# Performance work log

Measured on AMD Instinct MI355X. Metric: run time of the kernel, lower is better.

Reference implementation:

```python
import jax, jax.numpy as jnp
import numpy as np


def _lstm_step(h, c, x, W_ih, W_hh, b_ih, b_hh):
    # PyTorch gate order: i, f, g, o
    gates = x @ W_ih.T + b_ih + h @ W_hh.T + b_hh
    i, f, g, o = jnp.split(gates, 4, axis=-1)
    c = jax.nn.sigmoid(f) * c + jax.nn.sigmoid(i) * jnp.tanh(g)
    h = jax.nn.sigmoid(o) * jnp.tanh(c)
    return h, c


def setup_inputs() -> dict:
    key = jax.random.key(0)
    ks = jax.random.split(key, 12)
    B, T = 256, 256
    S, A, H, K = 64, 16, 512, 512
    D = S + A  # 80
    s = 1.0 / np.sqrt(H)
    u = lambda k, shape, sc: jax.random.uniform(k, shape, jnp.float32, -sc, sc)
    return {
        "traj": jax.random.normal(ks[0], (B, T, D), jnp.float32),
        "seq_len": T,
        "enc_W_ih": u(ks[1], (4 * H, D), s),
        "enc_W_hh": u(ks[2], (4 * H, H), s),
        "enc_b_ih": u(ks[3], (4 * H,), s),
        "enc_b_hh": u(ks[4], (4 * H,), s),
        "embeddings": jax.random.uniform(ks[5], (K, H), jnp.float32, -1.0 / K, 1.0 / K),
        "dec_W_ih": u(ks[6], (4 * H, D), s),
        "dec_W_hh": u(ks[7], (4 * H, H), s),
        "dec_b_ih": u(ks[8], (4 * H,), s),
        "dec_b_hh": u(ks[9], (4 * H,), s),
        "fc_W": u(ks[10], (D, H), s),
        "fc_b": u(ks[11], (D,), s),
    }


def reference(traj, seq_len, enc_W_ih, enc_W_hh, enc_b_ih, enc_b_hh,
              embeddings, dec_W_ih, dec_W_hh, dec_b_ih, dec_b_hh, fc_W, fc_b):
    B = traj.shape[0]
    H = enc_W_hh.shape[1]
    D = traj.shape[-1]

    # ---- Encoder: many-to-one LSTM, keep final hidden state ----
    def enc_step(carry, x_t):
        h, c = carry
        h, c = _lstm_step(h, c, x_t, enc_W_ih, enc_W_hh, enc_b_ih, enc_b_hh)
        return (h, c), None
    h0 = jnp.zeros((B, H), traj.dtype)
    (z, _), _ = jax.lax.scan(enc_step, (h0, h0), jnp.swapaxes(traj, 0, 1))

    # ---- Vector quantizer ----
    d = (jnp.sum(z * z, axis=1, keepdims=True)
         + jnp.sum(embeddings * embeddings, axis=1)
         - 2.0 * z @ embeddings.T)  # [B, K]
    idx = jnp.argmin(d, axis=1)
    quantized = embeddings[idx]  # [B, H]
    e_latent = jnp.mean((jax.lax.stop_gradient(quantized) - z) ** 2)
    q_latent = jnp.mean((quantized - jax.lax.stop_gradient(z)) ** 2)
    vq_loss = q_latent + 0.25 * e_latent

    def dec_step(carry, _):
        h, c, x = carry
        h, c = _lstm_step(h, c, x, dec_W_ih, dec_W_hh, dec_b_ih, dec_b_hh)
        y = h @ fc_W.T + fc_b
        return (h, c, y), y
    x0 = jnp.zeros((B, D), traj.dtype)
    c0 = jnp.zeros((B, H), traj.dtype)
    _, ys = jax.lax.scan(dec_step, (quantized, c0, x0), None, length=seq_len)
    recon = jnp.swapaxes(ys, 0, 1)  # [B, seq_len, D]
    return recon, vq_loss, idx[:, None]
```

## Files before the change

kernel.cpp:

```cpp
#include <hip/hip_runtime.h>
#include <math.h>

#define BB 256
#define TT 256
#define DDIM 80
#define HDIM 512
#define ROWSTRIDE 20480

#define WS_HA    0
#define WS_CD    131072
#define WS_BAR   262144
#define WS_HB    263168
#define WS_QUANT 394240
#define WS_VQP   525312
#define WS_BENC  525568
#define WS_BDEC0 527616
#define WS_BEFF  529664
#define WS_WEFF  531712

typedef _Float16 f16;
typedef f16 half4_t __attribute__((ext_vector_type(4)));
typedef f16 half8_t __attribute__((ext_vector_type(8)));
typedef float float4_t __attribute__((ext_vector_type(4)));

__device__ __forceinline__ float sigmoidf_(float v) { return 1.0f / (1.0f + expf(-v)); }

__device__ __forceinline__ void llc_store_f32(float* p, float v) {
  asm volatile("global_store_dword %0, %1, off sc0 sc1" :: "v"(p), "v"(v) : "memory");
}
__device__ __forceinline__ void llc_store_i32(int* p, int v) {
  asm volatile("global_store_dword %0, %1, off sc0 sc1" :: "v"(p), "v"(v) : "memory");
}
__device__ __forceinline__ int llc_load_i32(const int* p) {
  int v;
  asm volatile("global_load_dword %0, %1, off sc0 sc1\n\ts_waitcnt vmcnt(0)"
               : "=v"(v) : "v"(p) : "memory");
  return v;
}
__device__ __forceinline__ void wait_vm0() {
  asm volatile("s_waitcnt vmcnt(0)" ::: "memory");
}
__device__ __forceinline__ void llc_load_4xf4_cols(
    const float4* base,
    float4& a0, float4& a1, float4& a2, float4& a3) {
  asm volatile(
      "global_load_dwordx4 %0, %4, off sc0 sc1\n\t"
      "global_load_dwordx4 %1, %5, off sc0 sc1\n\t"
      "global_load_dwordx4 %2, %6, off sc0 sc1\n\t"
      "global_load_dwordx4 %3, %7, off sc0 sc1\n\t"
      "s_waitcnt vmcnt(0)"
      : "=&v"(a0), "=&v"(a1), "=&v"(a2), "=&v"(a3)
      : "v"(base), "v"(base + 32), "v"(base + 64), "v"(base + 96)
      : "memory");
}

__global__ __launch_bounds__(256) void zero_kernel(float4* __restrict__ p, int n4) {
  int i = blockIdx.x * 256 + threadIdx.x;
  if (i < n4) p[i] = make_float4(0.f, 0.f, 0.f, 0.f);
}

__global__ __launch_bounds__(256) void bias_init_kernel(
    const float* __restrict__ eb1, const float* __restrict__ eb2,
    const float* __restrict__ db1, const float* __restrict__ db2,
    const float* __restrict__ dWih, const float* __restrict__ fcb,
    float* __restrict__ b_enc, float* __restrict__ b_dec0,
    float* __restrict__ b_eff) {
  int n = blockIdx.x * 256 + threadIdx.x;
  b_enc[n] = eb1[n] + eb2[n];
  float bd = db1[n] + db2[n];
  b_dec0[n] = bd;
  float acc = bd;
  #pragma unroll 16
  for (int d = 0; d < DDIM; d++) acc += dWih[n * DDIM + d] * fcb[d];
  b_eff[n] = acc;
}

__global__ __launch_bounds__(256) void fold_kernel(
    const float* __restrict__ dWih, const float* __restrict__ dWhh,
    const float* __restrict__ fcW, float* __restrict__ W_eff) {
  int n = blockIdx.x;
  int tid = threadIdx.x;
  __shared__ float sw[DDIM];
  if (tid < DDIM) sw[tid] = dWih[n * DDIM + tid];
  __syncthreads();
  for (int k = tid; k < HDIM; k += 256) {
    float acc = dWhh[n * HDIM + k];
    #pragma unroll 16
    for (int d = 0; d < DDIM; d++) acc += sw[d] * fcW[d * HDIM + k];
    W_eff[n * HDIM + k] = acc;
  }
}

__global__ __launch_bounds__(256) void lstm_step_kernel(
    const float* __restrict__ Whh, const float* __restrict__ bias,
    const float* __restrict__ h_in, float* __restrict__ c,
    float* __restrict__ h_out) {
  __shared__ float sh[16][516];
  int tid = threadIdx.x;
  int rt = blockIdx.x & 15, jt = blockIdx.x >> 4;
  int row0 = rt << 4;
  for (int i = tid; i < 2048; i += 256) {
    int r = i >> 7, kq = i & 127;
    float4 v = *(const float4*)(h_in + (size_t)(row0 + r) * HDIM + (kq << 2));
    *(float4*)&sh[r][kq << 2] = v;
  }
  __syncthreads();
  int r = tid & 15, j0 = tid >> 4;
  int j = (jt << 4) + j0;
  float a0 = bias[j], a1 = bias[512 + j], a2 = bias[1024 + j], a3 = bias[1536 + j];
  const float4* w0 = (const float4*)(Whh + (size_t)j * HDIM);
  const float4* w1 = (const float4*)(Whh + (size_t)(512 + j) * HDIM);
  const float4* w2 = (const float4*)(Whh + (size_t)(1024 + j) * HDIM);
  const float4* w3 = (const float4*)(Whh + (size_t)(1536 + j) * HDIM);
  const float4* hv = (const float4*)&sh[r][0];
  #pragma unroll 4
  for (int kq = 0; kq < 128; kq++) {
    float4 h4 = hv[kq];
    float4 q0 = w0[kq], q1 = w1[kq], q2 = w2[kq], q3 = w3[kq];
    a0 += h4.x * q0.x + h4.y * q0.y + h4.z * q0.z + h4.w * q0.w;
    a1 += h4.x * q1.x + h4.y * q1.y + h4.z * q1.z + h4.w * q1.w;
    a2 += h4.x * q2.x + h4.y * q2.y + h4.z * q2.z + h4.w * q2.w;
    a3 += h4.x * q3.x + h4.y * q3.y + h4.z * q3.z + h4.w * q3.w;
  }
  size_t idx = (size_t)(row0 + r) * HDIM + j;
  float cv = c[idx];
  float cn = sigmoidf_(a1) * cv + sigmoidf_(a0) * tanhf(a2);
  float hn = sigmoidf_(a3) * tanhf(cn);
  c[idx] = cn;
  h_out[idx] = hn;
}

template <int IS_DEC>
__global__ __launch_bounds__(512, 2) void lstm_persist(
    const float* __restrict__ W,
    const float* __restrict__ Wih,
    const float* __restrict__ bias,
    const float* __restrict__ traj,
    const float* __restrict__ c_init,
    const float* __restrict__ fcW, const float* __restrict__ fcb,
    float* __restrict__ recon,
    float* __restrict__ hA, float* __restrict__ hB,
    int* __restrict__ flags) {
  constexpr int KT  = IS_DEC ? 16 : 19;
  constexpr int AST = IS_DEC ? 520 : 616;
  constexpr int RST = 132;
  __shared__ f16 Ahi[16 * AST];
  __shared__ f16 Alo[16 * AST];
  __shared__ float red[16 * RST];
  __shared__ float ypart[IS_DEC ? 8 * 260 : 4];

  const int tid = threadIdx.x;
  const int bid = blockIdx.x;
  const int rt = bid & 15, jt = bid >> 4;
  const int r0 = rt * 16, d0 = jt * 32;
  const int wv = __builtin_amdgcn_readfirstlane(tid >> 6);
  const int l15 = tid & 15;
  const int q = (tid >> 4) & 3;
  const int dh = wv >> 2, nt = wv & 3;

  #define SPLITC(vv, k) { \
    int off = (tid >> 5) * AST + (((tid & 31) + (k) * 32) << 2); \
    half4_t hi4, lo4; \
    float f0 = vv.x, f1 = vv.y, f2 = vv.z, f3 = vv.w; \
    f16 a = (f16)f0, b = (f16)f1, cc = (f16)f2, d = (f16)f3; \
    hi4[0] = a; hi4[1] = b; hi4[2] = cc; hi4[3] = d; \
    lo4[0] = (f16)(f0 - (float)a); lo4[1] = (f16)(f1 - (float)b); \
    lo4[2] = (f16)(f2 - (float)cc); lo4[3] = (f16)(f3 - (float)d); \
    *(half4_t*)&Ahi[off] = hi4; *(half4_t*)&Alo[off] = lo4; }

  const int grow = nt * 512 + d0 + dh * 16 + l15;
  half8_t Whi[KT], Wlo[KT];
  #pragma unroll
  for (int kt = 0; kt < KT; kt++) {
    #pragma unroll
    for (int j = 0; j < 8; j++) {
      int k = kt * 32 + q * 8 + j;
      float w;
      if (k < 512) w = W[(size_t)grow * HDIM + k];
      else {
        int kx = k - 512;
        w = (!IS_DEC && kx < DDIM) ? Wih[(size_t)grow * DDIM + kx] : 0.f;
      }
      f16 hi = (f16)w;
      Whi[kt][j] = hi;
      Wlo[kt][j] = (f16)(w - (float)hi);
    }
  }
  const float breg = bias[grow];

  half8_t Fhi[2], Flo[2];
  float ybias = 0.f;
  if (IS_DEC && jt < 5) {
    const int drow = jt * 16 + l15;
    #pragma unroll
    for (int kk = 0; kk < 2; kk++) {
      const int kt = wv * 2 + kk;
      #pragma unroll
      for (int j = 0; j < 8; j++) {
        float w = fcW[(size_t)drow * HDIM + kt * 32 + q * 8 + j];
        f16 hi = (f16)w;
        Fhi[kk][j] = hi;
        Flo[kk][j] = (f16)(w - (float)hi);
      }
    }
    ybias = fcb[jt * 16 + l15];
  }

  const int eb = tid >> 5, ed = tid & 31;
  float c_reg = IS_DEC ? c_init[(size_t)(r0 + eb) * HDIM + d0 + ed] : 0.f;
  __syncthreads();

  #define MFMA_RANGE(LO, HI) { \
    _Pragma("unroll") \
    for (int kt = (LO); kt < (HI); kt++) { \
      half8_t ahi = *(const half8_t*)&Ahi[abase + kt * 32]; \
      half8_t alo = *(const half8_t*)&Alo[abase + kt * 32]; \
      if (kt & 1) { \
        acc1 = __builtin_amdgcn_mfma_f32_16x16x32_f16(ahi, Whi[kt], acc1, 0, 0, 0); \
        acc1 = __builtin_amdgcn_mfma_f32_16x16x32_f16(alo, Whi[kt], acc1, 0, 0, 0); \
        acc1 = __builtin_amdgcn_mfma_f32_16x16x32_f16(ahi, Wlo[kt], acc1, 0, 0, 0); \
        acc1 = __builtin_amdgcn_mfma_f32_16x16x32_f16(alo, Wlo[kt], acc1, 0, 0, 0); \
      } else { \
        acc0 = __builtin_amdgcn_mfma_f32_16x16x32_f16(ahi, Whi[kt], acc0, 0, 0, 0); \
        acc0 = __builtin_amdgcn_mfma_f32_16x16x32_f16(alo, Whi[kt], acc0, 0, 0, 0); \
        acc0 = __builtin_amdgcn_mfma_f32_16x16x32_f16(ahi, Wlo[kt], acc0, 0, 0, 0); \
        acc0 = __builtin_amdgcn_mfma_f32_16x16x32_f16(alo, Wlo[kt], acc0, 0, 0, 0); \
      } \
    } }

  const int t_begin = IS_DEC ? 1 : 0;
  for (int t = t_begin; t < TT; t++) {
    const float* hin = (t & 1) ? hB : hA;
    float* hout = (t & 1) ? hA : hB;

    float4 xv0;
    if (!IS_DEC && tid < 384) {
      int row = tid / 24, c4 = tid % 24;
      xv0 = (c4 < 20)
          ? *(const float4*)(traj + (size_t)(r0 + row) * ROWSTRIDE +
                             (size_t)t * DDIM + c4 * 4)
          : make_float4(0.f, 0.f, 0.f, 0.f);
    }

    float4 v0, v1, v2, v3;
    const float4* base =
        (const float4*)(hin + (size_t)r0 * HDIM) + (tid >> 5) * 128 + (tid & 31);
    const bool is_t0 = (!IS_DEC && t == 0);
    if (!is_t0) {
      asm volatile(
          "global_load_dwordx4 %0, %4, off sc0 sc1\n\t"
          "global_load_dwordx4 %1, %5, off sc0 sc1\n\t"
          "global_load_dwordx4 %2, %6, off sc0 sc1\n\t"
          "global_load_dwordx4 %3, %7, off sc0 sc1"
          : "=&v"(v0), "=&v"(v1), "=&v"(v2), "=&v"(v3)
          : "v"(base), "v"(base + 32), "v"(base + 64), "v"(base + 96)
          : "memory");
      asm volatile("s_waitcnt vmcnt(2)" ::: "memory");
      __builtin_amdgcn_sched_barrier(0);
      SPLITC(v0, 0); SPLITC(v1, 1);
    } else {
      const int fo = (tid >> 5) * AST + ((tid & 31) << 4);
      uint4 z4; z4.x = 0; z4.y = 0; z4.z = 0; z4.w = 0;
      *(uint4*)&Ahi[fo] = z4; *(uint4*)&Ahi[fo + 8] = z4;
      *(uint4*)&Alo[fo] = z4; *(uint4*)&Alo[fo + 8] = z4;
    }
    __syncthreads();

    float4_t acc0 = {breg, breg, breg, breg};
    float4_t acc1 = {0.f, 0.f, 0.f, 0.f};
    const int abase = l15 * AST + q * 8;
    MFMA_RANGE(0, 8);

    if (!is_t0) {
      asm volatile("s_waitcnt vmcnt(0)" ::: "memory");
      __builtin_amdgcn_sched_barrier(0);
      SPLITC(v2, 2); SPLITC(v3, 3);
    }
    if (!IS_DEC && tid < 384) {
      int row = tid / 24, c4 = tid % 24;
      int off = row * AST + 512 + c4 * 4;
      half4_t hi4, lo4;
      float f0 = xv0.x, f1 = xv0.y, f2 = xv0.z, f3 = xv0.w;
      f16 a = (f16)f0, b = (f16)f1, cc = (f16)f2, d = (f16)f3;
      hi4[0] = a; hi4[1] = b; hi4[2] = cc; hi4[3] = d;
      lo4[0] = (f16)(f0 - (float)a); lo4[1] = (f16)(f1 - (float)b);
      lo4[2] = (f16)(f2 - (float)cc); lo4[3] = (f16)(f3 - (float)d);
      *(half4_t*)&Ahi[off] = hi4; *(half4_t*)&Alo[off] = lo4;
    }
    __syncthreads();
    MFMA_RANGE(8, KT);
    {
      float4_t C = acc0 + acc1;
      #pragma unroll
      for (int i = 0; i < 4; i++)
        red[(q * 4 + i) * RST + nt * 32 + dh * 16 + l15] = C[i];
    }
    __syncthreads();

    {
      float ig = red[eb * RST + ed];
      float fg = red[eb * RST + 32 + ed];
      float gg = red[eb * RST + 64 + ed];
      float og = red[eb * RST + 96 + ed];
      float cn = sigmoidf_(fg) * c_reg + sigmoidf_(ig) * tanhf(gg);
      c_reg = cn;
      llc_store_f32(&hout[(size_t)(r0 + eb) * HDIM + d0 + ed],
                    sigmoidf_(og) * tanhf(cn));
    }
    wait_vm0();
    __syncthreads();

    const int done = t - t_begin + 1;
    const bool do_bar = IS_DEC || t < TT - 1;
    if (do_bar && tid == 0) llc_store_i32(&flags[rt * 16 + jt], done);

    if (IS_DEC && jt < 5) {
      float4_t ya = {0.f, 0.f, 0.f, 0.f};
      #pragma unroll
      for (int kk = 0; kk < 2; kk++) {
        const int kt = wv * 2 + kk;
        const int ao = l15 * AST + kt * 32 + q * 8;
        half8_t ahi = *(const half8_t*)&Ahi[ao];
        half8_t alo = *(const half8_t*)&Alo[ao];
        ya = __builtin_amdgcn_mfma_f32_16x16x32_f16(ahi, Fhi[kk], ya, 0, 0, 0);
        ya = __builtin_amdgcn_mfma_f32_16x16x32_f16(alo, Fhi[kk], ya, 0, 0, 0);
        ya = __builtin_amdgcn_mfma_f32_16x16x32_f16(ahi, Flo[kk], ya, 0, 0, 0);
        ya = __builtin_amdgcn_mfma_f32_16x16x32_f16(alo, Flo[kk], ya, 0, 0, 0);
      }
      #pragma unroll
      for (int i = 0; i < 4; i++)
        ypart[wv * 260 + (q * 4 + i) * 16 + l15] = ya[i];
    }
    if (IS_DEC) __syncthreads();
    if (IS_DEC && jt < 5 && tid < 256) {
      float acc = ybias;
      #pragma unroll
      for (int w8 = 0; w8 < 8; w8++) acc += ypart[w8 * 260 + tid];
      recon[(size_t)(r0 + (tid >> 4)) * ROWSTRIDE + (size_t)(t - 1) * DDIM +
            jt * 16 + (tid & 15)] = acc;
    }

    if (do_bar) {
      if (tid < 64) {
        const int* fp = flags + rt * 16 + (tid & 15);
        while (llc_load_i32(fp) < done) {}
      }
      __syncthreads();
    }
  }

  if (IS_DEC) {
    if (jt >= 5) return;
    {
      const float4* base =
          (const float4*)(hA + (size_t)r0 * HDIM) + (tid >> 5) * 128 + (tid & 31);
      float4 v0, v1, v2, v3;
      llc_load_4xf4_cols(base, v0, v1, v2, v3);
      SPLITC(v0, 0); SPLITC(v1, 1); SPLITC(v2, 2); SPLITC(v3, 3);
    }
    __syncthreads();
    {
      float4_t ya = {0.f, 0.f, 0.f, 0.f};
      #pragma unroll
      for (int kk = 0; kk < 2; kk++) {
        const int kt = wv * 2 + kk;
        const int ao = l15 * AST + kt * 32 + q * 8;
        half8_t ahi = *(const half8_t*)&Ahi[ao];
        half8_t alo = *(const half8_t*)&Alo[ao];
        ya = __builtin_amdgcn_mfma_f32_16x16x32_f16(ahi, Fhi[kk], ya, 0, 0, 0);
        ya = __builtin_amdgcn_mfma_f32_16x16x32_f16(alo, Fhi[kk], ya, 0, 0, 0);
        ya = __builtin_amdgcn_mfma_f32_16x16x32_f16(ahi, Flo[kk], ya, 0, 0, 0);
        ya = __builtin_amdgcn_mfma_f32_16x16x32_f16(alo, Flo[kk], ya, 0, 0, 0);
      }
      #pragma unroll
      for (int i = 0; i < 4; i++)
        ypart[wv * 260 + (q * 4 + i) * 16 + l15] = ya[i];
    }
    __syncthreads();
    if (tid < 256) {
      float acc = ybias;
      #pragma unroll
      for (int w8 = 0; w8 < 8; w8++) acc += ypart[w8 * 260 + tid];
      recon[(size_t)(r0 + (tid >> 4)) * ROWSTRIDE + (size_t)255 * DDIM +
            jt * 16 + (tid & 15)] = acc;
    }
  }
  #undef SPLITC
  #undef MFMA_RANGE
}

__global__ __launch_bounds__(256) void vq_kernel(
    const float* __restrict__ z, const float* __restrict__ emb,
    float* __restrict__ quant, float* __restrict__ vq_part,
    float* __restrict__ out_idx) {
  __shared__ float sz[512];
  __shared__ float sd[256];
  __shared__ int si[256];
  int b = blockIdx.x, tid = threadIdx.x;
  sz[tid] = z[(size_t)b * HDIM + tid];
  sz[tid + 256] = z[(size_t)b * HDIM + 256 + tid];
  __syncthreads();
  float bd = 3.4e38f;
  int bk = 0;
  for (int k = tid; k < 512; k += 256) {
    const float4* e4 = (const float4*)(emb + (size_t)k * HDIM);
    const float4* z4 = (const float4*)sz;
    float dot = 0.f, ee = 0.f;
    #pragma unroll 4
    for (int qq = 0; qq < 128; qq++) {
      float4 ev = e4[qq], zv = z4[qq];
      dot += ev.x * zv.x + ev.y * zv.y + ev.z * zv.z + ev.w * zv.w;
      ee += ev.x * ev.x + ev.y * ev.y + ev.z * ev.z + ev.w * ev.w;
    }
    float dist = ee - 2.f * dot;
    if (dist < bd) { bd = dist; bk = k; }
  }
  sd[tid] = bd; si[tid] = bk;
  __syncthreads();
  for (int s = 128; s > 0; s >>= 1) {
    if (tid < s) {
      float od = sd[tid + s]; int ok = si[tid + s];
      if (od < sd[tid] || (od == sd[tid] && ok < si[tid])) { sd[tid] = od; si[tid] = ok; }
    }
    __syncthreads();
  }
  int kbest = si[0];
  __syncthreads();
  float e0 = emb[(size_t)kbest * HDIM + tid];
  float e1 = emb[(size_t)kbest * HDIM + 256 + tid];
  quant[(size_t)b * HDIM + tid] = e0;
  quant[(size_t)b * HDIM + 256 + tid] = e1;
  float q0 = e0 - sz[tid], q1 = e1 - sz[tid + 256];
  sd[tid] = q0 * q0 + q1 * q1;
  __syncthreads();
  for (int st = 128; st > 0; st >>= 1) {
    if (tid < st) sd[tid] += sd[tid + st];
    __syncthreads();
  }
  if (tid == 0) { vq_part[b] = sd[0]; out_idx[b] = (float)kbest; }
}

__global__ __launch_bounds__(256) void vq_reduce_kernel(const float* __restrict__ vq_part,
                                                        float* __restrict__ out_loss) {
  __shared__ float s[256];
  int tid = threadIdx.x;
  s[tid] = vq_part[tid];
  __syncthreads();
  for (int st = 128; st > 0; st >>= 1) {
    if (tid < st) s[tid] += s[tid + st];
    __syncthreads();
  }
  if (tid == 0) out_loss[0] = s[0] * 1.25f / (float)(BB * HDIM);
}

extern "C" void kernel_launch(void* const* d_in, const int* in_sizes, int n_in,
                              void* d_out, int out_size, void* d_ws, size_t ws_size,
                              hipStream_t stream) {
  const float* traj = (const float*)d_in[0];
  const float* eWih = (const float*)d_in[2];
  const float* eWhh = (const float*)d_in[3];
  const float* eb1  = (const float*)d_in[4];
  const float* eb2  = (const float*)d_in[5];
  const float* emb  = (const float*)d_in[6];
  const float* dWih = (const float*)d_in[7];
  const float* dWhh = (const float*)d_in[8];
  const float* db1  = (const float*)d_in[9];
  const float* db2  = (const float*)d_in[10];
  const float* fcW  = (const float*)d_in[11];
  const float* fcb  = (const float*)d_in[12];

  float* out = (float*)d_out;
  float* recon = out;
  float* out_loss = out + 5242880;
  float* out_idx = out + 5242881;

  float* ws = (float*)d_ws;
  float* hA      = ws + WS_HA;
  float* cD      = ws + WS_CD;
  int*   bar     = (int*)(ws + WS_BAR);
  float* hB      = ws + WS_HB;
  float* quant   = ws + WS_QUANT;
  float* vq_part = ws + WS_VQP;
  float* b_enc   = ws + WS_BENC;
  float* b_dec0  = ws + WS_BDEC0;
  float* b_eff   = ws + WS_BEFF;
  float* W_eff   = ws + WS_WEFF;

  zero_kernel<<<257, 256, 0, stream>>>((float4*)ws, 65792);
  bias_init_kernel<<<8, 256, 0, stream>>>(eb1, eb2, db1, db2, dWih, fcb,
                                          b_enc, b_dec0, b_eff);
  fold_kernel<<<2048, 256, 0, stream>>>(dWih, dWhh, fcW, W_eff);

  lstm_persist<0><<<256, 512, 0, stream>>>(
      eWhh, eWih, b_enc, traj, nullptr, nullptr, nullptr, nullptr, hA, hB, bar);

  vq_kernel<<<256, 256, 0, stream>>>(hA, emb, quant, vq_part, out_idx);
  vq_reduce_kernel<<<1, 256, 0, stream>>>(vq_part, out_loss);

  lstm_step_kernel<<<512, 256, 0, stream>>>(dWhh, b_dec0, quant, cD, hB);
  lstm_persist<1><<<256, 512, 0, stream>>>(
      W_eff, nullptr, b_eff, nullptr, cD, fcW, fcb, recon, hA, hB, bar + 256);
}
```

Baseline: 2.131 ms.

## Replace global step barrier with per-producer flag waits and trim split-precision MFMAs

Drops the all-to-all flag barrier at the end of each step. Each 32-thread group now waits only on the flag of the block that produced the 32 hidden columns it loads, then reads a contiguous 64-byte segment. The lo*lo MFMA term is removed, leaving three f16 products per tile instead of four, and the sigmoid/tanh calls are replaced with exp2/rcp intrinsic approximations. Together these cut synchronisation latency and per-step compute, at some cost in numerical accuracy. The previous overlap of the second half of the h load with the first MFMA range is removed.

New measurement: 2.179 ms. +2.3%, slower.

```diff
diff --git a/kernel.cpp b/kernel.cpp
--- a/kernel.cpp
+++ b/kernel.cpp
@@ -23,7 +23,12 @@
 typedef f16 half8_t __attribute__((ext_vector_type(8)));
 typedef float float4_t __attribute__((ext_vector_type(4)));
 
-__device__ __forceinline__ float sigmoidf_(float v) { return 1.0f / (1.0f + expf(-v)); }
+__device__ __forceinline__ float sigmoid_fast(float v) {
+  return __builtin_amdgcn_rcpf(1.0f + __builtin_amdgcn_exp2f(-1.44269504f * v));
+}
+__device__ __forceinline__ float tanh_fast(float v) {
+  return 2.0f * __builtin_amdgcn_rcpf(1.0f + __builtin_amdgcn_exp2f(-2.88539008f * v)) - 1.0f;
+}
 
 __device__ __forceinline__ void llc_store_f32(float* p, float v) {
   asm volatile("global_store_dword %0, %1, off sc0 sc1" :: "v"(p), "v"(v) : "memory");
@@ -40,17 +45,17 @@
 __device__ __forceinline__ void wait_vm0() {
   asm volatile("s_waitcnt vmcnt(0)" ::: "memory");
 }
-__device__ __forceinline__ void llc_load_4xf4_cols(
-    const float4* base,
-    float4& a0, float4& a1, float4& a2, float4& a3) {
+
+__device__ __forceinline__ void llc_load_64B(
+    const float* p, float4& a0, float4& a1, float4& a2, float4& a3) {
   asm volatile(
       "global_load_dwordx4 %0, %4, off sc0 sc1\n\t"
-      "global_load_dwordx4 %1, %5, off sc0 sc1\n\t"
-      "global_load_dwordx4 %2, %6, off sc0 sc1\n\t"
-      "global_load_dwordx4 %3, %7, off sc0 sc1\n\t"
+      "global_load_dwordx4 %1, %4, off offset:16 sc0 sc1\n\t"
+      "global_load_dwordx4 %2, %4, off offset:32 sc0 sc1\n\t"
+      "global_load_dwordx4 %3, %4, off offset:48 sc0 sc1\n\t"
       "s_waitcnt vmcnt(0)"
       : "=&v"(a0), "=&v"(a1), "=&v"(a2), "=&v"(a3)
-      : "v"(base), "v"(base + 32), "v"(base + 64), "v"(base + 96)
+      : "v"(p)
       : "memory");
 }
 
@@ -124,8 +129,8 @@
   }
   size_t idx = (size_t)(row0 + r) * HDIM + j;
   float cv = c[idx];
-  float cn = sigmoidf_(a1) * cv + sigmoidf_(a0) * tanhf(a2);
-  float hn = sigmoidf_(a3) * tanhf(cn);
+  float cn = sigmoid_fast(a1) * cv + sigmoid_fast(a0) * tanh_fast(a2);
+  float hn = sigmoid_fast(a3) * tanh_fast(cn);
   c[idx] = cn;
   h_out[idx] = hn;
 }
@@ -158,8 +163,12 @@
   const int q = (tid >> 4) & 3;
   const int dh = wv >> 2, nt = wv & 3;
 
-  #define SPLITC(vv, k) { \
-    int off = (tid >> 5) * AST + (((tid & 31) + (k) * 32) << 2); \
+  const int sp = tid >> 5;
+  const int sr = (tid & 31) >> 1;
+  const int scol = sp * 32 + (tid & 1) * 16;
+
+  #define SPLITC(vv, i) { \
+    int off = sr * AST + scol + (i) * 4; \
     half4_t hi4, lo4; \
     float f0 = vv.x, f1 = vv.y, f2 = vv.z, f3 = vv.w; \
     f16 a = (f16)f0, b = (f16)f1, cc = (f16)f2, d = (f16)f3; \
@@ -219,12 +228,10 @@
         acc1 = __builtin_amdgcn_mfma_f32_16x16x32_f16(ahi, Whi[kt], acc1, 0, 0, 0); \
         acc1 = __builtin_amdgcn_mfma_f32_16x16x32_f16(alo, Whi[kt], acc1, 0, 0, 0); \
         acc1 = __builtin_amdgcn_mfma_f32_16x16x32_f16(ahi, Wlo[kt], acc1, 0, 0, 0); \
-        acc1 = __builtin_amdgcn_mfma_f32_16x16x32_f16(alo, Wlo[kt], acc1, 0, 0, 0); \
       } else { \
         acc0 = __builtin_amdgcn_mfma_f32_16x16x32_f16(ahi, Whi[kt], acc0, 0, 0, 0); \
         acc0 = __builtin_amdgcn_mfma_f32_16x16x32_f16(alo, Whi[kt], acc0, 0, 0, 0); \
         acc0 = __builtin_amdgcn_mfma_f32_16x16x32_f16(ahi, Wlo[kt], acc0, 0, 0, 0); \
-        acc0 = __builtin_amdgcn_mfma_f32_16x16x32_f16(alo, Wlo[kt], acc0, 0, 0, 0); \
       } \
     } }
 
@@ -233,62 +240,40 @@
     const float* hin = (t & 1) ? hB : hA;
     float* hout = (t & 1) ? hA : hB;
 
-    float4 xv0;
     if (!IS_DEC && tid < 384) {
       int row = tid / 24, c4 = tid % 24;
-      xv0 = (c4 < 20)
+      float4 v = (c4 < 20)
           ? *(const float4*)(traj + (size_t)(r0 + row) * ROWSTRIDE +
                              (size_t)t * DDIM + c4 * 4)
           : make_float4(0.f, 0.f, 0.f, 0.f);
-    }
-
-    float4 v0, v1, v2, v3;
-    const float4* base =
-        (const float4*)(hin + (size_t)r0 * HDIM) + (tid >> 5) * 128 + (tid & 31);
-    const bool is_t0 = (!IS_DEC && t == 0);
-    if (!is_t0) {
-      asm volatile(
-          "global_load_dwordx4 %0, %4, off sc0 sc1\n\t"
-          "global_load_dwordx4 %1, %5, off sc0 sc1\n\t"
-          "global_load_dwordx4 %2, %6, off sc0 sc1\n\t"
-          "global_load_dwordx4 %3, %7, off sc0 sc1"
-          : "=&v"(v0), "=&v"(v1), "=&v"(v2), "=&v"(v3)
-          : "v"(base), "v"(base + 32), "v"(base + 64), "v"(base + 96)
-          : "memory");
-      asm volatile("s_waitcnt vmcnt(2)" ::: "memory");
-      __builtin_amdgcn_sched_barrier(0);
-      SPLITC(v0, 0); SPLITC(v1, 1);
-    } else {
-      const int fo = (tid >> 5) * AST + ((tid & 31) << 4);
-      uint4 z4; z4.x = 0; z4.y = 0; z4.z = 0; z4.w = 0;
-      *(uint4*)&Ahi[fo] = z4; *(uint4*)&Ahi[fo + 8] = z4;
-      *(uint4*)&Alo[fo] = z4; *(uint4*)&Alo[fo + 8] = z4;
-    }
-    __syncthreads();
-
-    float4_t acc0 = {breg, breg, breg, breg};
-    float4_t acc1 = {0.f, 0.f, 0.f, 0.f};
-    const int abase = l15 * AST + q * 8;
-    MFMA_RANGE(0, 8);
-
-    if (!is_t0) {
-      asm volatile("s_waitcnt vmcnt(0)" ::: "memory");
-      __builtin_amdgcn_sched_barrier(0);
-      SPLITC(v2, 2); SPLITC(v3, 3);
-    }
-    if (!IS_DEC && tid < 384) {
-      int row = tid / 24, c4 = tid % 24;
       int off = row * AST + 512 + c4 * 4;
       half4_t hi4, lo4;
-      float f0 = xv0.x, f1 = xv0.y, f2 = xv0.z, f3 = xv0.w;
+      float f0 = v.x, f1 = v.y, f2 = v.z, f3 = v.w;
       f16 a = (f16)f0, b = (f16)f1, cc = (f16)f2, d = (f16)f3;
       hi4[0] = a; hi4[1] = b; hi4[2] = cc; hi4[3] = d;
       lo4[0] = (f16)(f0 - (float)a); lo4[1] = (f16)(f1 - (float)b);
       lo4[2] = (f16)(f2 - (float)cc); lo4[3] = (f16)(f3 - (float)d);
       *(half4_t*)&Ahi[off] = hi4; *(half4_t*)&Alo[off] = lo4;
     }
-    __syncthreads();
-    MFMA_RANGE(8, KT);
+
+    {
+      const int thr = t - t_begin;
+      if (thr > 0 && (tid & 31) == 0) {
+        const int* fp = flags + rt * 16 + sp;
+        while (llc_load_i32(fp) < thr) {}
+      }
+      const float* hp = hin + (size_t)(r0 + sr) * HDIM + scol;
+      float4 v0, v1, v2, v3;
+      llc_load_64B(hp, v0, v1, v2, v3);
+      __builtin_amdgcn_sched_barrier(0);
+      SPLITC(v0, 0); SPLITC(v1, 1); SPLITC(v2, 2); SPLITC(v3, 3);
+    }
+    __syncthreads();
+
+    float4_t acc0 = {breg, breg, breg, breg};
+    float4_t acc1 = {0.f, 0.f, 0.f, 0.f};
+    const int abase = l15 * AST + q * 8;
+    MFMA_RANGE(0, KT);
     {
       float4_t C = acc0 + acc1;
       #pragma unroll
@@ -302,17 +287,17 @@
       float fg = red[eb * RST + 32 + ed];
       float gg = red[eb * RST + 64 + ed];
       float og = red[eb * RST + 96 + ed];
-      float cn = sigmoidf_(fg) * c_reg + sigmoidf_(ig) * tanhf(gg);
+      float cn = sigmoid_fast(fg) * c_reg + sigmoid_fast(ig) * tanh_fast(gg);
       c_reg = cn;
       llc_store_f32(&hout[(size_t)(r0 + eb) * HDIM + d0 + ed],
-                    sigmoidf_(og) * tanhf(cn));
+                    sigmoid_fast(og) * tanh_fast(cn));
     }
     wait_vm0();
     __syncthreads();
 
     const int done = t - t_begin + 1;
-    const bool do_bar = IS_DEC || t < TT - 1;
-    if (do_bar && tid == 0) llc_store_i32(&flags[rt * 16 + jt], done);
+    if ((IS_DEC || t < TT - 1) && tid == 0)
+      llc_store_i32(&flags[rt * 16 + jt], done);
 
     if (IS_DEC && jt < 5) {
       float4_t ya = {0.f, 0.f, 0.f, 0.f};
@@ -330,32 +315,28 @@
       #pragma unroll
       for (int i = 0; i < 4; i++)
         ypart[wv * 260 + (q * 4 + i) * 16 + l15] = ya[i];
-    }
-    if (IS_DEC) __syncthreads();
-    if (IS_DEC && jt < 5 && tid < 256) {
-      float acc = ybias;
-      #pragma unroll
-      for (int w8 = 0; w8 < 8; w8++) acc += ypart[w8 * 260 + tid];
-      recon[(size_t)(r0 + (tid >> 4)) * ROWSTRIDE + (size_t)(t - 1) * DDIM +
-            jt * 16 + (tid & 15)] = acc;
-    }
-
-    if (do_bar) {
-      if (tid < 64) {
-        const int* fp = flags + rt * 16 + (tid & 15);
-        while (llc_load_i32(fp) < done) {}
-      }
       __syncthreads();
+      if (tid < 256) {
+        float acc = ybias;
+        #pragma unroll
+        for (int w8 = 0; w8 < 8; w8++) acc += ypart[w8 * 260 + tid];
+        recon[(size_t)(r0 + (tid >> 4)) * ROWSTRIDE + (size_t)(t - 1) * DDIM +
+              jt * 16 + (tid & 15)] = acc;
+      }
     }
   }
 
   if (IS_DEC) {
     if (jt >= 5) return;
     {
-      const float4* base =
-          (const float4*)(hA + (size_t)r0 * HDIM) + (tid >> 5) * 128 + (tid & 31);
+      if ((tid & 31) == 0) {
+        const int* fp = flags + rt * 16 + sp;
+        while (llc_load_i32(fp) < 255) {}
+      }
+      const float* hp = hA + (size_t)(r0 + sr) * HDIM + scol;
       float4 v0, v1, v2, v3;
-      llc_load_4xf4_cols(base, v0, v1, v2, v3);
+      llc_load_64B(hp, v0, v1, v2, v3);
+      __builtin_amdgcn_sched_barrier(0);
       SPLITC(v0, 0); SPLITC(v1, 1); SPLITC(v2, 2); SPLITC(v3, 3);
     }
     __syncthreads();
```
